# Kernel optimization log

Hardware: AMD Instinct MI355X
Metric: run time of the kernel (lower is better)

Reference implementation:

```python
import jax, jax.numpy as jnp
import numpy as np

B, D, K = 32768, 1024, 64
N3, N4, N5 = 512, 512, 512


def setup_inputs() -> dict:
    key = jax.random.key(0)
    ks = jax.random.split(key, 10)
    # x in [-1, 1]^D as the docstring states
    x = jax.random.uniform(ks[0], (B, D), dtype=jnp.float32, minval=-1.0, maxval=1.0)
    S = jnp.sort(jax.random.randint(ks[1], (K,), 0, D, dtype=jnp.int32))
    a = jax.random.normal(ks[2], (K,), dtype=jnp.float32)
    b = jax.random.normal(ks[3], (K, K), dtype=jnp.float32)
    idx3 = jax.random.randint(ks[4], (N3, 3), 0, K, dtype=jnp.int32)
    c3 = jax.random.normal(ks[5], (N3,), dtype=jnp.float32)
    idx4 = jax.random.randint(ks[6], (N4, 4), 0, K, dtype=jnp.int32)
    c4 = jax.random.normal(ks[7], (N4,), dtype=jnp.float32)
    idx5 = jax.random.randint(ks[8], (N5, 5), 0, K, dtype=jnp.int32)
    c5 = jax.random.normal(ks[9], (N5,), dtype=jnp.float32)
    return {"x": x, "S": S, "a": a, "b": b, "idx3": idx3, "c3": c3,
            "idx4": idx4, "c4": c4, "idx5": idx5, "c5": c5}


def _monomial_term(xS, idx, c):
    # xS: (B,k); idx: (n,deg); c: (n,) -> (B,)
    # gather -> (B, n, deg), product over monomial factors, weighted sum
    prod = jnp.prod(xS[:, idx], axis=2)  # (B, n)
    return prod @ c


def reference(x, S, a, b, idx3, c3, idx4, c4, idx5, c5):
    xS = x[:, S]                      # (B, k)
    lin = xS @ a                      # (B,)
    # sum_{i<j} b[i,j] xS_i xS_j == einsum with strictly-upper-triangular b
    bu = jnp.triu(b, k=1)             # (k, k)
    quad = jnp.einsum('bi,ij,bj->b', xS, bu, xS)
    out = lin + quad
    out = out + _monomial_term(xS, idx3, c3)
    out = out + _monomial_term(xS, idx4, c4)
    out = out + _monomial_term(xS, idx5, c5)
    return out
```

## Files before the change

kernel.cpp:

```cpp
#include <hip/hip_runtime.h>
#include <stdint.h>

#define NT 256
#define RPB 16
#define XSTR 80

#define WS_TAB   0
#define TB_P3    0
#define TB_P4    4096
#define TB_P5    8192
#define TB_P5E   12288
#define TB_C4    13312
#define TB_C5    14336
#define TB_SZ    15360
#define WS_BUT   15360
#define WS_CGCOL 31744
#define WS_CGSL  32000
#define WS_LEAD  32512

static __device__ __forceinline__ unsigned short f2bf(float f) {
    unsigned u = __float_as_uint(f);
    return (unsigned short)((u + 0x7FFFu + ((u >> 16) & 1u)) >> 16);
}
static __device__ __forceinline__ float bf2f(unsigned short h) {
    return __uint_as_float((unsigned)h << 16);
}
static __device__ __forceinline__ float4 f4fma(float s, float4 v, float4 acc) {
    acc.x += s * v.x; acc.y += s * v.y; acc.z += s * v.z; acc.w += s * v.w;
    return acc;
}

__global__ void prepack(const int* __restrict__ S, const float* __restrict__ b,
                        const int* __restrict__ i3, const float* __restrict__ c3,
                        const int* __restrict__ i4, const float* __restrict__ c4,
                        const int* __restrict__ i5, const float* __restrict__ c5,
                        unsigned char* __restrict__ ws)
{
    __shared__ short slotS[1024];
    __shared__ int cnt;
    const int tid = threadIdx.x;
    for (int e = tid; e < 1024; e += NT) slotS[e] = -1;
    if (tid == 0) cnt = 0;
    __syncthreads();
    if (tid < 64) {
        int sv = S[tid];
        int k0 = tid;
        while (k0 > 0 && S[k0 - 1] == sv) --k0;
        ((short*)(ws + WS_LEAD))[tid] = (short)k0;
        if (k0 == tid) slotS[sv] = (short)tid;
    }
    __syncthreads();
    int* cgcol = (int*)(ws + WS_CGCOL);
    short4* cgsl = (short4*)(ws + WS_CGSL);
    {
        int g = tid;
        short s0 = slotS[4*g], s1 = slotS[4*g+1], s2 = slotS[4*g+2], s3 = slotS[4*g+3];
        if (s0 >= 0 || s1 >= 0 || s2 >= 0 || s3 >= 0) {
            int pos = atomicAdd(&cnt, 1);
            cgcol[pos] = g;
            cgsl[pos] = make_short4(s0 >= 0 ? (short)(s0 * XSTR) : (short)-1,
                                    s1 >= 0 ? (short)(s1 * XSTR) : (short)-1,
                                    s2 >= 0 ? (short)(s2 * XSTR) : (short)-1,
                                    s3 >= 0 ? (short)(s3 * XSTR) : (short)-1);
        }
    }
    __syncthreads();
    if (tid == 0) {
        for (int p = cnt; p < 64; ++p) {
            cgcol[p] = 0;
            cgsl[p] = make_short4(-1, -1, -1, -1);
        }
    }
    float* buT = (float*)(ws + WS_BUT);
    for (int e = tid; e < 4096; e += NT) {
        int j = e >> 6, i = e & 63;
        buT[e] = (i < j) ? b[i * 64 + j] : 0.0f;
    }
    ushort4* p3 = (ushort4*)(ws + TB_P3);
    ushort4* p4 = (ushort4*)(ws + TB_P4);
    ushort4* p5 = (ushort4*)(ws + TB_P5);
    unsigned short* p5e = (unsigned short*)(ws + TB_P5E);
    unsigned short* c4h = (unsigned short*)(ws + TB_C4);
    unsigned short* c5h = (unsigned short*)(ws + TB_C5);
    for (int t = tid; t < 512; t += NT) {
        p3[t] = make_ushort4((unsigned short)(i3[3*t+0]*XSTR), (unsigned short)(i3[3*t+1]*XSTR),
                             (unsigned short)(i3[3*t+2]*XSTR), f2bf(c3[t]));
        p4[t] = make_ushort4((unsigned short)(i4[4*t+0]*XSTR), (unsigned short)(i4[4*t+1]*XSTR),
                             (unsigned short)(i4[4*t+2]*XSTR), (unsigned short)(i4[4*t+3]*XSTR));
        p5[t] = make_ushort4((unsigned short)(i5[5*t+0]*XSTR), (unsigned short)(i5[5*t+1]*XSTR),
                             (unsigned short)(i5[5*t+2]*XSTR), (unsigned short)(i5[5*t+3]*XSTR));
        p5e[t] = (unsigned short)(i5[5*t+4]*XSTR);
        c4h[t] = f2bf(c4[t]);
        c5h[t] = f2bf(c5[t]);
    }
}

__global__ __launch_bounds__(NT, 6)
void poly_main(const float* __restrict__ x, const float* __restrict__ a,
               const unsigned char* __restrict__ ws, float* __restrict__ out)
{
    __shared__ float xS[64 * 20];
    __shared__ unsigned char tabL[TB_SZ];
    __shared__ float red[64];

    const int tid  = threadIdx.x;
    const int row0 = blockIdx.x * RPB;

    {
        const uint4* src = (const uint4*)(ws + WS_TAB);
        uint4* dst = (uint4*)tabL;
        for (int e = tid; e < TB_SZ / 16; e += NT) dst[e] = src[e];
    }
    {
        const int g = tid & 63, rs = tid >> 6;
        int col4 = ((const int*)(ws + WS_CGCOL))[g];
        short4 sl = ((const short4*)(ws + WS_CGSL))[g];
        if (sl.x >= 0 || sl.y >= 0 || sl.z >= 0 || sl.w >= 0) {
            const float4* Xrow = (const float4*)(x + (size_t)row0 * 1024);
            char* xsb = (char*)xS;
            #pragma unroll
            for (int m = 0; m < 4; ++m) {
                int r = rs * 4 + m;
                float4 v = Xrow[r * 256 + col4];
                int rb = r * 4;
                if (sl.x >= 0) *(float*)(xsb + sl.x + rb) = v.x;
                if (sl.y >= 0) *(float*)(xsb + sl.y + rb) = v.y;
                if (sl.z >= 0) *(float*)(xsb + sl.z + rb) = v.z;
                if (sl.w >= 0) *(float*)(xsb + sl.w + rb) = v.w;
            }
        }
    }
    __syncthreads();
    {
        int k = tid >> 2, q = tid & 3;
        int k0 = ((const short*)(ws + WS_LEAD))[k];
        if (k0 != k) {
            float4* dst = (float4*)((char*)xS + k  * XSTR);
            const float4* src = (const float4*)((char*)xS + k0 * XSTR);
            dst[q] = src[q];
        }
    }
    __syncthreads();

    const int rg = tid & 3;
    const int ts = tid >> 2;
    const char* xb = (const char*)xS + rg * 16;

    float4 d = make_float4(0.f, 0.f, 0.f, 0.f);
    {
        const float4* buT4 = (const float4*)(ws + WS_BUT) + ts * 16;
        const int nii = (ts + 3) >> 2;
        #pragma unroll 4
        for (int ii = 0; ii < nii; ++ii) {
            float4 bb  = buT4[ii];
            float4 xi0 = *(const float4*)(xb + (ii * 4 + 0) * XSTR);
            float4 xi1 = *(const float4*)(xb + (ii * 4 + 1) * XSTR);
            float4 xi2 = *(const float4*)(xb + (ii * 4 + 2) * XSTR);
            float4 xi3 = *(const float4*)(xb + (ii * 4 + 3) * XSTR);
            d = f4fma(bb.x, xi0, d);
            d = f4fma(bb.y, xi1, d);
            d = f4fma(bb.z, xi2, d);
            d = f4fma(bb.w, xi3, d);
        }
    }
    float av = a[ts];
    float4 xj = *(const float4*)(xb + ts * XSTR);
    float4 acc;
    acc.x = (av + d.x) * xj.x;
    acc.y = (av + d.y) * xj.y;
    acc.z = (av + d.z) * xj.z;
    acc.w = (av + d.w) * xj.w;

    const ushort4* p3L = (const ushort4*)(tabL + TB_P3);
    const ushort4* p4L = (const ushort4*)(tabL + TB_P4);
    const ushort4* p5L = (const ushort4*)(tabL + TB_P5);
    const unsigned short* p5eL = (const unsigned short*)(tabL + TB_P5E);
    const unsigned short* c4L  = (const unsigned short*)(tabL + TB_C4);
    const unsigned short* c5L  = (const unsigned short*)(tabL + TB_C5);

    #pragma unroll 4
    for (int m = 0; m < 8; ++m) {
        ushort4 p = p3L[64 * m + ts];
        float4 v0 = *(const float4*)(xb + p.x);
        float4 v1 = *(const float4*)(xb + p.y);
        float4 v2 = *(const float4*)(xb + p.z);
        float c = bf2f(p.w);
        acc.x += c * ((v0.x * v1.x) * v2.x);
        acc.y += c * ((v0.y * v1.y) * v2.y);
        acc.z += c * ((v0.z * v1.z) * v2.z);
        acc.w += c * ((v0.w * v1.w) * v2.w);
    }
    #pragma unroll 2
    for (int m = 0; m < 8; ++m) {
        int t = 64 * m + ts;
        ushort4 p = p4L[t];
        float c = bf2f(c4L[t]);
        float4 v0 = *(const float4*)(xb + p.x);
        float4 v1 = *(const float4*)(xb + p.y);
        float4 v2 = *(const float4*)(xb + p.z);
        float4 v3 = *(const float4*)(xb + p.w);
        acc.x += c * ((v0.x * v1.x) * (v2.x * v3.x));
        acc.y += c * ((v0.y * v1.y) * (v2.y * v3.y));
        acc.z += c * ((v0.z * v1.z) * (v2.z * v3.z));
        acc.w += c * ((v0.w * v1.w) * (v2.w * v3.w));
    }
    #pragma unroll 2
    for (int m = 0; m < 8; ++m) {
        int t = 64 * m + ts;
        ushort4 p = p5L[t];
        int o4 = p5eL[t];
        float c = bf2f(c5L[t]);
        float4 v0 = *(const float4*)(xb + p.x);
        float4 v1 = *(const float4*)(xb + p.y);
        float4 v2 = *(const float4*)(xb + p.z);
        float4 v3 = *(const float4*)(xb + p.w);
        float4 v4 = *(const float4*)(xb + o4);
        acc.x += c * (((v0.x * v1.x) * (v2.x * v3.x)) * v4.x);
        acc.y += c * (((v0.y * v1.y) * (v2.y * v3.y)) * v4.y);
        acc.z += c * (((v0.z * v1.z) * (v2.z * v3.z)) * v4.z);
        acc.w += c * (((v0.w * v1.w) * (v2.w * v3.w)) * v4.w);
    }

    #pragma unroll
    for (int mask = 4; mask <= 32; mask <<= 1) {
        acc.x += __shfl_xor(acc.x, mask, 64);
        acc.y += __shfl_xor(acc.y, mask, 64);
        acc.z += __shfl_xor(acc.z, mask, 64);
        acc.w += __shfl_xor(acc.w, mask, 64);
    }
    const int w = tid >> 6;
    const int lane = tid & 63;
    if (lane < 4) ((float4*)red)[w * 4 + lane] = acc;
    __syncthreads();
    if (tid < 16) {
        float s = red[tid] + red[16 + tid] + red[32 + tid] + red[48 + tid];
        out[row0 + tid] = s;
    }
}

extern "C" void kernel_launch(void* const* d_in, const int* in_sizes, int n_in,
                              void* d_out, int out_size, void* d_ws, size_t ws_size,
                              hipStream_t stream) {
    const float* x  = (const float*)d_in[0];
    const int*   S  = (const int*)d_in[1];
    const float* a  = (const float*)d_in[2];
    const float* b  = (const float*)d_in[3];
    const int*   i3 = (const int*)d_in[4];
    const float* c3 = (const float*)d_in[5];
    const int*   i4 = (const int*)d_in[6];
    const float* c4 = (const float*)d_in[7];
    const int*   i5 = (const int*)d_in[8];
    const float* c5 = (const float*)d_in[9];
    unsigned char* ws = (unsigned char*)d_ws;
    float* out = (float*)d_out;

    prepack<<<1, NT, 0, stream>>>(S, b, i3, c3, i4, c4, i5, c5, ws);
    poly_main<<<32768 / RPB, NT, 0, stream>>>(x, a, ws, out);
}
```

Before: 230.9 us.

## Read monomial tables from global memory and gather xS with scalar loads

Stops staging the 15 KB monomial index/coefficient table into LDS and instead reads packed uint2/uint4 entries straight from global memory (cached) in the inner loops. The x gather becomes a simple per-column scalar load using S directly, replacing the deduplicated float4 column-group scheme and the duplicate-fixup pass. Prepack now runs on 16 blocks, and the launch bound drops to 4 waves per SIMD while unroll factors rise. The aim is to cut LDS traffic and prologue cost per block, at the price of uncoalesced scalar x loads and global-cache reads of the tables.

New measurement: 213.3 us. -7.6%, faster.

```diff
diff --git a/kernel.cpp b/kernel.cpp
--- a/kernel.cpp
+++ b/kernel.cpp
@@ -5,139 +5,68 @@
 #define RPB 16
 #define XSTR 80
 
-#define WS_TAB   0
-#define TB_P3    0
-#define TB_P4    4096
-#define TB_P5    8192
-#define TB_P5E   12288
-#define TB_C4    13312
-#define TB_C5    14336
-#define TB_SZ    15360
-#define WS_BUT   15360
-#define WS_CGCOL 31744
-#define WS_CGSL  32000
-#define WS_LEAD  32512
+#define WS_P3   0
+#define WS_P4   4096
+#define WS_P5   12288
+#define WS_BUT  20480
 
 static __device__ __forceinline__ unsigned short f2bf(float f) {
     unsigned u = __float_as_uint(f);
     return (unsigned short)((u + 0x7FFFu + ((u >> 16) & 1u)) >> 16);
 }
-static __device__ __forceinline__ float bf2f(unsigned short h) {
-    return __uint_as_float((unsigned)h << 16);
+static __device__ __forceinline__ float bfbits(unsigned lo16) {
+    return __uint_as_float(lo16 << 16);
 }
 static __device__ __forceinline__ float4 f4fma(float s, float4 v, float4 acc) {
     acc.x += s * v.x; acc.y += s * v.y; acc.z += s * v.z; acc.w += s * v.w;
     return acc;
 }
 
-__global__ void prepack(const int* __restrict__ S, const float* __restrict__ b,
+__global__ void prepack(const float* __restrict__ b,
                         const int* __restrict__ i3, const float* __restrict__ c3,
                         const int* __restrict__ i4, const float* __restrict__ c4,
                         const int* __restrict__ i5, const float* __restrict__ c5,
                         unsigned char* __restrict__ ws)
 {
-    __shared__ short slotS[1024];
-    __shared__ int cnt;
-    const int tid = threadIdx.x;
-    for (int e = tid; e < 1024; e += NT) slotS[e] = -1;
-    if (tid == 0) cnt = 0;
-    __syncthreads();
-    if (tid < 64) {
-        int sv = S[tid];
-        int k0 = tid;
-        while (k0 > 0 && S[k0 - 1] == sv) --k0;
-        ((short*)(ws + WS_LEAD))[tid] = (short)k0;
-        if (k0 == tid) slotS[sv] = (short)tid;
+    const int g = blockIdx.x * NT + threadIdx.x;
+    float* buT = (float*)(ws + WS_BUT);
+    if (g < 4096) {
+        int j = g >> 6, i = g & 63;
+        buT[g] = (i < j) ? b[i * 64 + j] : 0.0f;
     }
-    __syncthreads();
-    int* cgcol = (int*)(ws + WS_CGCOL);
-    short4* cgsl = (short4*)(ws + WS_CGSL);
-    {
-        int g = tid;
-        short s0 = slotS[4*g], s1 = slotS[4*g+1], s2 = slotS[4*g+2], s3 = slotS[4*g+3];
-        if (s0 >= 0 || s1 >= 0 || s2 >= 0 || s3 >= 0) {
-            int pos = atomicAdd(&cnt, 1);
-            cgcol[pos] = g;
-            cgsl[pos] = make_short4(s0 >= 0 ? (short)(s0 * XSTR) : (short)-1,
-                                    s1 >= 0 ? (short)(s1 * XSTR) : (short)-1,
-                                    s2 >= 0 ? (short)(s2 * XSTR) : (short)-1,
-                                    s3 >= 0 ? (short)(s3 * XSTR) : (short)-1);
-        }
-    }
-    __syncthreads();
-    if (tid == 0) {
-        for (int p = cnt; p < 64; ++p) {
-            cgcol[p] = 0;
-            cgsl[p] = make_short4(-1, -1, -1, -1);
-        }
-    }
-    float* buT = (float*)(ws + WS_BUT);
-    for (int e = tid; e < 4096; e += NT) {
-        int j = e >> 6, i = e & 63;
-        buT[e] = (i < j) ? b[i * 64 + j] : 0.0f;
-    }
-    ushort4* p3 = (ushort4*)(ws + TB_P3);
-    ushort4* p4 = (ushort4*)(ws + TB_P4);
-    ushort4* p5 = (ushort4*)(ws + TB_P5);
-    unsigned short* p5e = (unsigned short*)(ws + TB_P5E);
-    unsigned short* c4h = (unsigned short*)(ws + TB_C4);
-    unsigned short* c5h = (unsigned short*)(ws + TB_C5);
-    for (int t = tid; t < 512; t += NT) {
-        p3[t] = make_ushort4((unsigned short)(i3[3*t+0]*XSTR), (unsigned short)(i3[3*t+1]*XSTR),
-                             (unsigned short)(i3[3*t+2]*XSTR), f2bf(c3[t]));
-        p4[t] = make_ushort4((unsigned short)(i4[4*t+0]*XSTR), (unsigned short)(i4[4*t+1]*XSTR),
-                             (unsigned short)(i4[4*t+2]*XSTR), (unsigned short)(i4[4*t+3]*XSTR));
-        p5[t] = make_ushort4((unsigned short)(i5[5*t+0]*XSTR), (unsigned short)(i5[5*t+1]*XSTR),
-                             (unsigned short)(i5[5*t+2]*XSTR), (unsigned short)(i5[5*t+3]*XSTR));
-        p5e[t] = (unsigned short)(i5[5*t+4]*XSTR);
-        c4h[t] = f2bf(c4[t]);
-        c5h[t] = f2bf(c5[t]);
+    if (g < 512) {
+        unsigned o0, o1, o2, o3, o4;
+        o0 = (unsigned)i3[3*g+0] * XSTR; o1 = (unsigned)i3[3*g+1] * XSTR; o2 = (unsigned)i3[3*g+2] * XSTR;
+        ((uint2*)(ws + WS_P3))[g] = make_uint2(o0 | (o1 << 16), o2 | ((unsigned)f2bf(c3[g]) << 16));
+        o0 = (unsigned)i4[4*g+0] * XSTR; o1 = (unsigned)i4[4*g+1] * XSTR;
+        o2 = (unsigned)i4[4*g+2] * XSTR; o3 = (unsigned)i4[4*g+3] * XSTR;
+        ((uint4*)(ws + WS_P4))[g] = make_uint4(o0 | (o1 << 16), o2 | (o3 << 16), (unsigned)f2bf(c4[g]), 0u);
+        o0 = (unsigned)i5[5*g+0] * XSTR; o1 = (unsigned)i5[5*g+1] * XSTR;
+        o2 = (unsigned)i5[5*g+2] * XSTR; o3 = (unsigned)i5[5*g+3] * XSTR;
+        o4 = (unsigned)i5[5*g+4] * XSTR;
+        ((uint4*)(ws + WS_P5))[g] = make_uint4(o0 | (o1 << 16), o2 | (o3 << 16), o4 | ((unsigned)f2bf(c5[g]) << 16), 0u);
     }
 }
 
-__global__ __launch_bounds__(NT, 6)
-void poly_main(const float* __restrict__ x, const float* __restrict__ a,
+__global__ __launch_bounds__(NT, 4)
+void poly_main(const float* __restrict__ x, const int* __restrict__ S,
+               const float* __restrict__ a,
                const unsigned char* __restrict__ ws, float* __restrict__ out)
 {
-    __shared__ float xS[64 * 20];
-    __shared__ unsigned char tabL[TB_SZ];
+    __shared__ __align__(16) float xS[64 * 20];
     __shared__ float red[64];
 
     const int tid  = threadIdx.x;
     const int row0 = blockIdx.x * RPB;
 
     {
-        const uint4* src = (const uint4*)(ws + WS_TAB);
-        uint4* dst = (uint4*)tabL;
-        for (int e = tid; e < TB_SZ / 16; e += NT) dst[e] = src[e];
-    }
-    {
-        const int g = tid & 63, rs = tid >> 6;
-        int col4 = ((const int*)(ws + WS_CGCOL))[g];
-        short4 sl = ((const short4*)(ws + WS_CGSL))[g];
-        if (sl.x >= 0 || sl.y >= 0 || sl.z >= 0 || sl.w >= 0) {
-            const float4* Xrow = (const float4*)(x + (size_t)row0 * 1024);
-            char* xsb = (char*)xS;
-            #pragma unroll
-            for (int m = 0; m < 4; ++m) {
-                int r = rs * 4 + m;
-                float4 v = Xrow[r * 256 + col4];
-                int rb = r * 4;
-                if (sl.x >= 0) *(float*)(xsb + sl.x + rb) = v.x;
-                if (sl.y >= 0) *(float*)(xsb + sl.y + rb) = v.y;
-                if (sl.z >= 0) *(float*)(xsb + sl.z + rb) = v.z;
-                if (sl.w >= 0) *(float*)(xsb + sl.w + rb) = v.w;
-            }
-        }
-    }
-    __syncthreads();
-    {
-        int k = tid >> 2, q = tid & 3;
-        int k0 = ((const short*)(ws + WS_LEAD))[k];
-        if (k0 != k) {
-            float4* dst = (float4*)((char*)xS + k  * XSTR);
-            const float4* src = (const float4*)((char*)xS + k0 * XSTR);
-            dst[q] = src[q];
+        const int k = tid & 63, q = tid >> 6;
+        const int sk = S[k];
+        const float* xc = x + (size_t)row0 * 1024 + sk;
+        #pragma unroll
+        for (int m = 0; m < 4; ++m) {
+            int r = q * 4 + m;
+            xS[k * 20 + r] = xc[(size_t)r * 1024];
         }
     }
     __syncthreads();
@@ -163,7 +92,7 @@
             d = f4fma(bb.w, xi3, d);
         }
     }
-    float av = a[ts];
+    const float av = a[ts];
     float4 xj = *(const float4*)(xb + ts * XSTR);
     float4 acc;
     acc.x = (av + d.x) * xj.x;
@@ -171,50 +100,44 @@
     acc.z = (av + d.z) * xj.z;
     acc.w = (av + d.w) * xj.w;
 
-    const ushort4* p3L = (const ushort4*)(tabL + TB_P3);
-    const ushort4* p4L = (const ushort4*)(tabL + TB_P4);
-    const ushort4* p5L = (const ushort4*)(tabL + TB_P5);
-    const unsigned short* p5eL = (const unsigned short*)(tabL + TB_P5E);
-    const unsigned short* c4L  = (const unsigned short*)(tabL + TB_C4);
-    const unsigned short* c5L  = (const unsigned short*)(tabL + TB_C5);
+    const uint2* p3 = (const uint2*)(ws + WS_P3);
+    const uint4* p4 = (const uint4*)(ws + WS_P4);
+    const uint4* p5 = (const uint4*)(ws + WS_P5);
 
     #pragma unroll 4
     for (int m = 0; m < 8; ++m) {
-        ushort4 p = p3L[64 * m + ts];
-        float4 v0 = *(const float4*)(xb + p.x);
-        float4 v1 = *(const float4*)(xb + p.y);
-        float4 v2 = *(const float4*)(xb + p.z);
-        float c = bf2f(p.w);
+        uint2 p = p3[64 * m + ts];
+        float4 v0 = *(const float4*)(xb + (p.x & 0xFFFFu));
+        float4 v1 = *(const float4*)(xb + (p.x >> 16));
+        float4 v2 = *(const float4*)(xb + (p.y & 0xFFFFu));
+        float c = bfbits(p.y >> 16);
         acc.x += c * ((v0.x * v1.x) * v2.x);
         acc.y += c * ((v0.y * v1.y) * v2.y);
         acc.z += c * ((v0.z * v1.z) * v2.z);
         acc.w += c * ((v0.w * v1.w) * v2.w);
     }
-    #pragma unroll 2
+    #pragma unroll 4
     for (int m = 0; m < 8; ++m) {
-        int t = 64 * m + ts;
-        ushort4 p = p4L[t];
-        float c = bf2f(c4L[t]);
-        float4 v0 = *(const float4*)(xb + p.x);
-        float4 v1 = *(const float4*)(xb + p.y);
-        float4 v2 = *(const float4*)(xb + p.z);
-        float4 v3 = *(const float4*)(xb + p.w);
+        uint4 p = p4[64 * m + ts];
+        float4 v0 = *(const float4*)(xb + (p.x & 0xFFFFu));
+        float4 v1 = *(const float4*)(xb + (p.x >> 16));
+        float4 v2 = *(const float4*)(xb + (p.y & 0xFFFFu));
+        float4 v3 = *(const float4*)(xb + (p.y >> 16));
+        float c = bfbits(p.z & 0xFFFFu);
         acc.x += c * ((v0.x * v1.x) * (v2.x * v3.x));
         acc.y += c * ((v0.y * v1.y) * (v2.y * v3.y));
         acc.z += c * ((v0.z * v1.z) * (v2.z * v3.z));
         acc.w += c * ((v0.w * v1.w) * (v2.w * v3.w));
     }
-    #pragma unroll 2
+    #pragma unroll 4
     for (int m = 0; m < 8; ++m) {
-        int t = 64 * m + ts;
-        ushort4 p = p5L[t];
-        int o4 = p5eL[t];
-        float c = bf2f(c5L[t]);
-        float4 v0 = *(const float4*)(xb + p.x);
-        float4 v1 = *(const float4*)(xb + p.y);
-        float4 v2 = *(const float4*)(xb + p.z);
-        float4 v3 = *(const float4*)(xb + p.w);
-        float4 v4 = *(const float4*)(xb + o4);
+        uint4 p = p5[64 * m + ts];
+        float4 v0 = *(const float4*)(xb + (p.x & 0xFFFFu));
+        float4 v1 = *(const float4*)(xb + (p.x >> 16));
+        float4 v2 = *(const float4*)(xb + (p.y & 0xFFFFu));
+        float4 v3 = *(const float4*)(xb + (p.y >> 16));
+        float4 v4 = *(const float4*)(xb + (p.z & 0xFFFFu));
+        float c = bfbits(p.z >> 16);
         acc.x += c * (((v0.x * v1.x) * (v2.x * v3.x)) * v4.x);
         acc.y += c * (((v0.y * v1.y) * (v2.y * v3.y)) * v4.y);
         acc.z += c * (((v0.z * v1.z) * (v2.z * v3.z)) * v4.z);
@@ -228,13 +151,11 @@
         acc.z += __shfl_xor(acc.z, mask, 64);
         acc.w += __shfl_xor(acc.w, mask, 64);
     }
-    const int w = tid >> 6;
-    const int lane = tid & 63;
+    const int w = tid >> 6, lane = tid & 63;
     if (lane < 4) ((float4*)red)[w * 4 + lane] = acc;
     __syncthreads();
     if (tid < 16) {
-        float s = red[tid] + red[16 + tid] + red[32 + tid] + red[48 + tid];
-        out[row0 + tid] = s;
+        out[row0 + tid] = red[tid] + red[16 + tid] + red[32 + tid] + red[48 + tid];
     }
 }
 
@@ -254,6 +175,6 @@
     unsigned char* ws = (unsigned char*)d_ws;
     float* out = (float*)d_out;
 
-    prepack<<<1, NT, 0, stream>>>(S, b, i3, c3, i4, c4, i5, c5, ws);
-    poly_main<<<32768 / RPB, NT, 0, stream>>>(x, a, ws, out);
+    prepack<<<16, NT, 0, stream>>>(b, i3, c3, i4, c4, i5, c5, ws);
+    poly_main<<<32768 / RPB, NT, 0, stream>>>(x, S, a, ws, out);
 }
```
